# Performance work log

Measured on AMD Instinct MI355X. Metric: run time of the kernel, lower is better.

Reference implementation:

```python
import jax, jax.numpy as jnp
import numpy as np

NUM_TREES = 150
ARITY = 4
DEPTH = 4
NUM_LEVELS = DEPTH + 1  # leaves (level 0) ... root (level DEPTH)
VOCAB = 10000
SUBTOK = 8
EMB_DIM = 256
HID = 256
NUM_CLASSES = 2


def _build_forest():
    # perfect ARITY-ary tree, level-order indexing; edges point child -> parent
    n = (ARITY ** (DEPTH + 1) - 1) // (ARITY - 1)  # 341
    src = np.arange(1, n)
    dst = (src - 1) // ARITY
    depth_of = np.zeros(n, dtype=np.int64)
    for j in range(1, n):
        depth_of[j] = depth_of[(j - 1) // ARITY] + 1
    level_of = DEPTH - depth_of  # leaves = 0, processed first (topo order)
    offs = np.arange(NUM_TREES) * n
    edge_src = (src[None, :] + offs[:, None]).ravel().astype(np.int32)
    edge_dst = (dst[None, :] + offs[:, None]).ravel().astype(np.int32)
    node_level = np.tile(level_of, NUM_TREES).astype(np.int32)
    graph_id = np.repeat(np.arange(NUM_TREES), n).astype(np.int32)
    leaf_mask = (node_level == 0).astype(np.int32)
    return edge_src, edge_dst, node_level, graph_id, leaf_mask, NUM_TREES * n


def setup_inputs() -> dict:
    key = jax.random.key(0)
    ks = jax.random.split(key, 16)
    es, ed, lvl, gid, lm, N = _build_forest()
    s_e = 1.0 / np.sqrt(EMB_DIM)
    s_h = 1.0 / np.sqrt(HID)
    s_f = 1.0 / np.sqrt(2 * HID)
    return {
        "node_feat1": jax.random.randint(ks[0], (N, SUBTOK), 0, VOCAB, dtype=jnp.int32),
        "node_feat2": jax.random.randint(ks[1], (N, SUBTOK), 0, VOCAB, dtype=jnp.int32),
        "emb1": jax.random.normal(ks[2], (VOCAB, EMB_DIM), jnp.float32) * 0.02,
        "emb2": jax.random.normal(ks[3], (VOCAB, EMB_DIM), jnp.float32) * 0.02,
        "W_iou1": jax.random.normal(ks[4], (EMB_DIM, 3 * HID), jnp.float32) * s_e,
        "W_iou2": jax.random.normal(ks[5], (EMB_DIM, 3 * HID), jnp.float32) * s_e,
        "U_iou1": jax.random.normal(ks[6], (HID, 3 * HID), jnp.float32) * s_h,
        "U_iou2": jax.random.normal(ks[7], (HID, 3 * HID), jnp.float32) * s_h,
        "Uf_W1": jax.random.normal(ks[8], (HID, HID), jnp.float32) * s_h,
        "Uf_b1": jnp.zeros((HID,), jnp.float32),
        "Uf_W2": jax.random.normal(ks[9], (HID, HID), jnp.float32) * s_h,
        "Uf_b2": jnp.zeros((HID,), jnp.float32),
        "b_iou1": jnp.zeros((3 * HID,), jnp.float32),
        "b_iou2": jnp.zeros((3 * HID,), jnp.float32),
        "Wf": jax.random.normal(ks[10], (2 * HID, NUM_CLASSES), jnp.float32) * s_f,
        "bf": jnp.zeros((NUM_CLASSES,), jnp.float32),
        "edge_src": jnp.asarray(es),
        "edge_dst": jnp.asarray(ed),
        "node_level": jnp.asarray(lvl),
        "graph_id": jnp.asarray(gid),
        "leaf_mask": jnp.asarray(lm),
    }


def _tree_lstm(iou0, U_iou, Uf_W, Uf_b, b_iou, edge_src, edge_dst, node_level):
    # ChildSum TreeLSTM, propagated level-by-level (leaves -> root)
    N = iou0.shape[0]
    h = jnp.zeros((N, HID), iou0.dtype)
    c = jnp.zeros((N, HID), iou0.dtype)
    for lvl in range(NUM_LEVELS):
        emask = (node_level[edge_dst] == lvl).astype(h.dtype)[:, None]  # [E,1]
        hs = h[edge_src] * emask  # children h (already computed at lower levels)
        f = jax.nn.sigmoid(hs @ Uf_W + Uf_b)  # per-edge forget gate
        h_tild = jax.ops.segment_sum(hs, edge_dst, num_segments=N)
        c_sum = jax.ops.segment_sum(f * c[edge_src] * emask, edge_dst, num_segments=N)
        has_child = jax.ops.segment_sum(emask, edge_dst, num_segments=N) > 0  # [N,1]
        # DGL semantics: reduce overwrites iou for internal nodes; leaves keep W_iou(x)*mask
        iou = jnp.where(has_child, h_tild @ U_iou, iou0) + b_iou
        i, o, u = jnp.split(iou, 3, axis=1)
        c_new = jax.nn.sigmoid(i) * jnp.tanh(u) + c_sum
        h_new = jax.nn.sigmoid(o) * jnp.tanh(c_new)
        at = (node_level == lvl)[:, None]
        h = jnp.where(at, h_new, h)
        c = jnp.where(at, c_new, c)
    return h


def _branch(node_feat, emb, W_iou, U_iou, Uf_W, Uf_b, b_iou,
            leaf_mask, edge_src, edge_dst, node_level, graph_id):
    embeds = emb[node_feat].mean(axis=1)  # subtoken mean pooling -> [N, EMB_DIM]
    iou0 = (embeds @ W_iou) * leaf_mask.astype(embeds.dtype)[:, None]
    h = _tree_lstm(iou0, U_iou, Uf_W, Uf_b, b_iou, edge_src, edge_dst, node_level)
    s = jax.ops.segment_sum(h, graph_id, num_segments=NUM_TREES)
    cnt = jax.ops.segment_sum(jnp.ones((h.shape[0],), h.dtype), graph_id, num_segments=NUM_TREES)
    return jax.nn.relu(s / cnt[:, None])  # mean graph readout + relu


def reference(node_feat1, node_feat2, emb1, emb2, W_iou1, W_iou2, U_iou1, U_iou2,
              Uf_W1, Uf_b1, Uf_W2, Uf_b2, b_iou1, b_iou2, Wf, bf,
              edge_src, edge_dst, node_level, graph_id, leaf_mask):
    m1 = _branch(node_feat1, emb1, W_iou1, U_iou1, Uf_W1, Uf_b1, b_iou1,
                 leaf_mask, edge_src, edge_dst, node_level, graph_id)
    m2 = _branch(node_feat2, emb2, W_iou2, U_iou2, Uf_W2, Uf_b2, b_iou2,
                 leaf_mask, edge_src, edge_dst, node_level, graph_id)
    logits = jax.nn.leaky_relu(jnp.concatenate([m1, m2], axis=1) @ Wf + bf, 0.01)
    return jax.nn.softmax(logits, axis=-1)
```

## Files before the change

kernel.cpp:

```cpp
#include <hip/hip_runtime.h>

#define NT 150
#define NPT 341
#define LEAF0 85
#define NL (NT*256)
#define NN (NT*NPT)
#define VOCAB 10000

typedef __attribute__((ext_vector_type(8))) short short8;
typedef __attribute__((ext_vector_type(4))) float floatx4;

__device__ __forceinline__ float sigf(float x){ return 1.0f/(1.0f+__expf(-x)); }
__device__ __forceinline__ float bf2f(ushort u){ union{unsigned i; float f;} v; v.i = ((unsigned)u)<<16; return v.f; }
__device__ __forceinline__ ushort f2bf(float x){ union{float f; unsigned i;} v; v.f = x; return (ushort)((v.i + 0x7fff + ((v.i>>16)&1))>>16); }

__global__ __launch_bounds__(256) void convW_k(
    const float* __restrict__ W1, const float* __restrict__ U1, const float* __restrict__ F1,
    const float* __restrict__ W2, const float* __restrict__ U2, const float* __restrict__ F2,
    ushort* Wt1, ushort* Ut1, ushort* Ft1, ushort* Wt2, ushort* Ut2, ushort* Ft2){
  __shared__ float T[32][33];
  const float* src; ushort* dst; int N;
  switch (blockIdx.z){
    case 0: src=W1; dst=Wt1; N=768; break;
    case 1: src=U1; dst=Ut1; N=768; break;
    case 2: src=F1; dst=Ft1; N=256; break;
    case 3: src=W2; dst=Wt2; N=768; break;
    case 4: src=U2; dst=Ut2; N=768; break;
    default: src=F2; dst=Ft2; N=256; break;
  }
  int n0 = blockIdx.x*32; if (n0 >= N) return;
  int k0 = blockIdx.y*32;
  int nl = threadIdx.x & 31, kb = threadIdx.x >> 5;
  #pragma unroll
  for (int i=0;i<4;i++){ int kk = kb*4+i; T[kk][nl] = src[(size_t)(k0+kk)*N + n0 + nl]; }
  __syncthreads();
  #pragma unroll
  for (int i=0;i<4;i++){ int nn = kb*4+i; dst[(size_t)(n0+nn)*256 + k0 + nl] = f2bf(T[nl][nn]); }
}

__global__ __launch_bounds__(256) void convE_k(
    const float* __restrict__ e1, const float* __restrict__ e2,
    ushort* __restrict__ E1, ushort* __restrict__ E2){
  const float* s = blockIdx.y ? e2 : e1;
  ushort* d = blockIdx.y ? E2 : E1;
  size_t i = ((size_t)blockIdx.x*256 + threadIdx.x)*4;
  float4 v = *(const float4*)&s[i];
  d[i+0]=f2bf(v.x); d[i+1]=f2bf(v.y); d[i+2]=f2bf(v.z); d[i+3]=f2bf(v.w);
}

__global__ __launch_bounds__(256) void embed_k(
    const int* __restrict__ f1, const int* __restrict__ f2,
    const ushort* __restrict__ E1, const ushort* __restrict__ E2,
    ushort* __restrict__ h1, ushort* __restrict__ h2){
  int br = blockIdx.y;
  const int* feat = br ? f2 : f1;
  const ushort* E = br ? E2 : E1;
  ushort* h = br ? h2 : h1;
  int t = threadIdx.x;
  int leaf = blockIdx.x*16 + (t>>4);
  int seg = t & 15;
  int tree = leaf >> 8;
  size_t node = (size_t)tree*NPT + LEAF0 + (leaf & 255);
  const int* f = feat + node*8;
  float s[16];
  #pragma unroll
  for (int q=0;q<16;q++) s[q]=0.f;
  #pragma unroll
  for (int j=0;j<8;j++){
    const ushort* row = E + (size_t)f[j]*256 + seg*16;
    short8 a = *(const short8*)row;
    short8 b = *(const short8*)(row+8);
    #pragma unroll
    for (int q=0;q<8;q++){ s[q]+=bf2f((ushort)a[q]); s[8+q]+=bf2f((ushort)b[q]); }
  }
  short8 o1, o2;
  #pragma unroll
  for (int q=0;q<8;q++){ o1[q]=(short)f2bf(s[q]*0.125f); o2[q]=(short)f2bf(s[8+q]*0.125f); }
  ushort* dst = h + node*256 + seg*16;
  *(short8*)dst = o1; *(short8*)(dst+8) = o2;
}

__global__ __launch_bounds__(1024) void leaf_gemm(
    const ushort* __restrict__ Wt1, const float* __restrict__ b1,
    const ushort* __restrict__ Wt2, const float* __restrict__ b2,
    ushort* __restrict__ h1, ushort* __restrict__ c1,
    ushort* __restrict__ h2, ushort* __restrict__ c2){
  __shared__ __attribute__((aligned(16))) ushort As[8][64*40];
  int br = blockIdx.y;
  const ushort* Wt = br ? Wt2 : Wt1;
  const float* biou = br ? b2 : b1;
  ushort* h = br ? h2 : h1;
  ushort* c = br ? c2 : c1;
  int tid = threadIdx.x;
  int lane = tid & 63, wav = tid >> 6, quad = lane >> 4, l15 = lane & 15;
  int rowbase = blockIdx.x*64;

  {
    int row = tid >> 4, seg = tid & 15;
    int leaf = rowbase + row;
    int tree = leaf >> 8;
    size_t node = (size_t)tree*NPT + LEAF0 + (leaf & 255);
    const ushort* src = h + node*256 + seg*16;
    short8 a = *(const short8*)src;
    short8 b = *(const short8*)(src+8);
    int cch = seg >> 1, off = (seg & 1)*16;
    *(short8*)&As[cch][row*40 + off]     = a;
    *(short8*)&As[cch][row*40 + off + 8] = b;
  }
  __syncthreads();

  floatx4 acc[3][4];
  #pragma unroll
  for (int g=0;g<3;g++)
    #pragma unroll
    for (int r=0;r<4;r++) acc[g][r] = (floatx4){0.f,0.f,0.f,0.f};

  const ushort* bp0 = Wt + (size_t)(0*256 + wav*16 + l15)*256 + quad*8;
  const ushort* bp1 = Wt + (size_t)(1*256 + wav*16 + l15)*256 + quad*8;
  const ushort* bp2 = Wt + (size_t)(2*256 + wav*16 + l15)*256 + quad*8;

  #pragma unroll
  for (int cch=0; cch<8; cch++){
    short8 b0 = *(const short8*)(bp0 + cch*32);
    short8 b1 = *(const short8*)(bp1 + cch*32);
    short8 b2 = *(const short8*)(bp2 + cch*32);
    #pragma unroll
    for (int r=0;r<4;r++){
      short8 a = *(const short8*)&As[cch][(16*r + l15)*40 + quad*8];
      acc[0][r] = __builtin_amdgcn_mfma_f32_16x16x32_bf16(a, b0, acc[0][r], 0,0,0);
      acc[1][r] = __builtin_amdgcn_mfma_f32_16x16x32_bf16(a, b1, acc[1][r], 0,0,0);
      acc[2][r] = __builtin_amdgcn_mfma_f32_16x16x32_bf16(a, b2, acc[2][r], 0,0,0);
    }
  }
  int hc = wav*16 + l15;
  float bi = biou[hc], bo = biou[256+hc], bu = biou[512+hc];
  #pragma unroll
  for (int r=0;r<4;r++){
    #pragma unroll
    for (int reg=0;reg<4;reg++){
      int leaf = rowbase + 16*r + quad*4 + reg;
      int tree = leaf >> 8;
      size_t node = (size_t)tree*NPT + LEAF0 + (leaf & 255);
      float iv = acc[0][r][reg] + bi;
      float ov = acc[1][r][reg] + bo;
      float uv = acc[2][r][reg] + bu;
      float cc = sigf(iv)*tanhf(uv);
      float hh = sigf(ov)*tanhf(cc);
      h[node*256 + hc] = f2bf(hh);
      c[node*256 + hc] = f2bf(cc);
    }
  }
}

__global__ __launch_bounds__(256) void level_k(
    const ushort* __restrict__ Ut1, const ushort* __restrict__ Ft1,
    const float* __restrict__ Ufb1, const float* __restrict__ bi1,
    const ushort* __restrict__ Ut2, const ushort* __restrict__ Ft2,
    const float* __restrict__ Ufb2, const float* __restrict__ bi2,
    ushort* __restrict__ h1, ushort* __restrict__ c1,
    ushort* __restrict__ h2, ushort* __restrict__ c2,
    int M, int shift, int base){
  __shared__ __attribute__((aligned(16))) ushort Ch[8][64*40];
  __shared__ __attribute__((aligned(16))) ushort Ht[8][16*40];
  __shared__ float Cs[16*68];
  int br = blockIdx.z;
  const ushort* Ut = br ? Ut2 : Ut1;
  const ushort* Ft = br ? Ft2 : Ft1;
  const float* Ufb = br ? Ufb2 : Ufb1;
  const float* biou = br ? bi2 : bi1;
  ushort* h = br ? h2 : h1;
  ushort* c = br ? c2 : c1;
  int tid = threadIdx.x;
  int lane = tid & 63, wav = tid >> 6, quad = lane >> 4, l15 = lane & 15;
  int m0 = blockIdx.x*16, cb = blockIdx.y;
  int mask = (1<<shift)-1;

  {
    int cl = tid >> 2, q4 = tid & 3;
    int sm = m0 + (cl >> 2); if (sm > M-1) sm = M-1;
    int stree = sm >> shift, sloc = base + (sm & mask);
    const ushort* sgp = h + ((size_t)stree*NPT + 4*sloc + 1 + (cl & 3))*256 + q4*8;
    #pragma unroll
    for (int cc=0;cc<8;cc++)
      *(short8*)&Ch[cc][cl*40 + q4*8] = *(const short8*)(sgp + cc*32);
  }
  __syncthreads();
  {
    int n = tid & 15, hcki = tid >> 4;
    int cc = hcki >> 1, off = (hcki & 1)*16;
    float s[16];
    #pragma unroll
    for (int q=0;q<16;q++) s[q]=0.f;
    #pragma unroll
    for (int i=0;i<4;i++){
      short8 a = *(const short8*)&Ch[cc][(4*n+i)*40 + off];
      short8 b = *(const short8*)&Ch[cc][(4*n+i)*40 + off + 8];
      #pragma unroll
      for (int q=0;q<8;q++){ s[q]+=bf2f((ushort)a[q]); s[8+q]+=bf2f((ushort)b[q]); }
    }
    short8 o1,o2;
    #pragma unroll
    for (int q=0;q<8;q++){ o1[q]=(short)f2bf(s[q]); o2[q]=(short)f2bf(s[8+q]); }
    *(short8*)&Ht[cc][n*40 + off]     = o1;
    *(short8*)&Ht[cc][n*40 + off + 8] = o2;
  }
  __syncthreads();

  const ushort* bfp = Ft + (size_t)(cb*64 + wav*16 + l15)*256 + quad*8;
  const ushort* bp0 = Ut + (size_t)(0*256 + cb*64 + wav*16 + l15)*256 + quad*8;
  const ushort* bp1 = Ut + (size_t)(1*256 + cb*64 + wav*16 + l15)*256 + quad*8;
  const ushort* bp2 = Ut + (size_t)(2*256 + cb*64 + wav*16 + l15)*256 + quad*8;

  floatx4 accf[4], acci[3];
  #pragma unroll
  for (int r=0;r<4;r++) accf[r] = (floatx4){0.f,0.f,0.f,0.f};
  #pragma unroll
  for (int g=0;g<3;g++) acci[g] = (floatx4){0.f,0.f,0.f,0.f};

  #pragma unroll
  for (int cc=0; cc<8; cc++){
    short8 bfw = *(const short8*)(bfp + cc*32);
    short8 b0 = *(const short8*)(bp0 + cc*32);
    short8 b1 = *(const short8*)(bp1 + cc*32);
    short8 b2 = *(const short8*)(bp2 + cc*32);
    short8 ah = *(const short8*)&Ht[cc][l15*40 + quad*8];
    #pragma unroll
    for (int r=0;r<4;r++){
      short8 a = *(const short8*)&Ch[cc][(16*r + l15)*40 + quad*8];
      accf[r] = __builtin_amdgcn_mfma_f32_16x16x32_bf16(a, bfw, accf[r], 0,0,0);
    }
    acci[0] = __builtin_amdgcn_mfma_f32_16x16x32_bf16(ah, b0, acci[0], 0,0,0);
    acci[1] = __builtin_amdgcn_mfma_f32_16x16x32_bf16(ah, b1, acci[1], 0,0,0);
    acci[2] = __builtin_amdgcn_mfma_f32_16x16x32_bf16(ah, b2, acci[2], 0,0,0);
  }

  int hc = cb*64 + wav*16 + l15;
  float ufb = Ufb[hc];
  #pragma unroll
  for (int r=0;r<4;r++){
    int ni = 4*r + quad;
    int m = m0 + ni; if (m > M-1) m = M-1;
    int tree = m >> shift, loc = base + (m & mask);
    size_t chbase = ((size_t)tree*NPT + 4*loc + 1)*256 + hc;
    float cs = 0.f;
    #pragma unroll
    for (int reg=0;reg<4;reg++)
      cs += sigf(accf[r][reg] + ufb) * bf2f(c[chbase + (size_t)reg*256]);
    Cs[ni*68 + wav*16 + l15] = cs;
  }
  __syncthreads();
  float bi = biou[hc], bo = biou[256+hc], bu = biou[512+hc];
  #pragma unroll
  for (int reg=0;reg<4;reg++){
    int ni = quad*4 + reg;
    int m = m0 + ni;
    if (m < M){
      int tree = m >> shift, loc = base + (m & mask);
      size_t off = ((size_t)tree*NPT + loc)*256 + hc;
      float cs = Cs[ni*68 + wav*16 + l15];
      float iv = acci[0][reg] + bi;
      float ov = acci[1][reg] + bo;
      float uv = acci[2][reg] + bu;
      float cn = sigf(iv)*tanhf(uv) + cs;
      float hn = sigf(ov)*tanhf(cn);
      h[off] = f2bf(hn);
      c[off] = f2bf(cn);
    }
  }
}

__global__ __launch_bounds__(256) void readout_k(
    const ushort* __restrict__ h1, const ushort* __restrict__ h2,
    float* __restrict__ m1, float* __restrict__ m2){
  int br = blockIdx.y;
  const ushort* h = br ? h2 : h1;
  float* mo = br ? m2 : m1;
  int tree = blockIdx.x; int t = threadIdx.x;
  const ushort* hp = h + (size_t)tree*NPT*256 + t;
  float s0=0.f,s1=0.f,s2=0.f,s3=0.f;
  for (int i=0; i<340; i+=4){
    s0 += bf2f(hp[(size_t)(i+0)*256]); s1 += bf2f(hp[(size_t)(i+1)*256]);
    s2 += bf2f(hp[(size_t)(i+2)*256]); s3 += bf2f(hp[(size_t)(i+3)*256]);
  }
  float s = s0+s1+s2+s3 + bf2f(hp[(size_t)340*256]);
  mo[tree*256+t] = fmaxf(s*(1.0f/341.0f), 0.f);
}

__global__ __launch_bounds__(64) void final_k(const float* __restrict__ m1,
    const float* __restrict__ m2, const float* __restrict__ Wf,
    const float* __restrict__ bf, float* __restrict__ out){
  int tree = blockIdx.x; int t = threadIdx.x;
  float p0=0.f, p1=0.f;
  for (int k=t;k<512;k+=64){
    float x = (k<256) ? m1[tree*256+k] : m2[tree*256+(k-256)];
    p0 += x*Wf[k*2+0]; p1 += x*Wf[k*2+1];
  }
  #pragma unroll
  for (int off=32; off>0; off>>=1){
    p0 += __shfl_down(p0, off);
    p1 += __shfl_down(p1, off);
  }
  if (t==0){
    float l0 = p0+bf[0], l1 = p1+bf[1];
    l0 = (l0>0.f)?l0:0.01f*l0;
    l1 = (l1>0.f)?l1:0.01f*l1;
    float mx = fmaxf(l0,l1);
    float e0 = __expf(l0-mx), e1 = __expf(l1-mx);
    float inv = 1.0f/(e0+e1);
    out[tree*2+0] = e0*inv; out[tree*2+1] = e1*inv;
  }
}

extern "C" void kernel_launch(void* const* d_in, const int* in_sizes, int n_in,
                              void* d_out, int out_size, void* d_ws, size_t ws_size,
                              hipStream_t stream) {
  const int*   feat1 = (const int*)  d_in[0];
  const int*   feat2 = (const int*)  d_in[1];
  const float* emb1  = (const float*)d_in[2];
  const float* emb2  = (const float*)d_in[3];
  const float* Wiou1 = (const float*)d_in[4];
  const float* Wiou2 = (const float*)d_in[5];
  const float* Uiou1 = (const float*)d_in[6];
  const float* Uiou2 = (const float*)d_in[7];
  const float* UfW1  = (const float*)d_in[8];
  const float* Ufb1  = (const float*)d_in[9];
  const float* UfW2  = (const float*)d_in[10];
  const float* Ufb2  = (const float*)d_in[11];
  const float* biou1 = (const float*)d_in[12];
  const float* biou2 = (const float*)d_in[13];
  const float* Wf    = (const float*)d_in[14];
  const float* bfv   = (const float*)d_in[15];
  float* out = (float*)d_out;

  char* ws = (char*)d_ws;
  ushort* h1  = (ushort*)ws;  ws += (size_t)NN*256*2;
  ushort* h2  = (ushort*)ws;  ws += (size_t)NN*256*2;
  ushort* c1  = (ushort*)ws;  ws += (size_t)NN*256*2;
  ushort* c2  = (ushort*)ws;  ws += (size_t)NN*256*2;
  ushort* E1  = (ushort*)ws;  ws += (size_t)VOCAB*256*2;
  ushort* E2  = (ushort*)ws;  ws += (size_t)VOCAB*256*2;
  ushort* Wt1 = (ushort*)ws;  ws += 768*256*2;
  ushort* Ut1 = (ushort*)ws;  ws += 768*256*2;
  ushort* Ft1 = (ushort*)ws;  ws += 256*256*2;
  ushort* Wt2 = (ushort*)ws;  ws += 768*256*2;
  ushort* Ut2 = (ushort*)ws;  ws += 768*256*2;
  ushort* Ft2 = (ushort*)ws;  ws += 256*256*2;
  float*  m1  = (float*)ws;   ws += NT*256*4;
  float*  m2  = (float*)ws;   ws += NT*256*4;

  convW_k<<<dim3(24, 8, 6), 256, 0, stream>>>(Wiou1, Uiou1, UfW1, Wiou2, Uiou2, UfW2,
                                              Wt1, Ut1, Ft1, Wt2, Ut2, Ft2);
  convE_k<<<dim3(2500, 2), 256, 0, stream>>>(emb1, emb2, E1, E2);
  embed_k<<<dim3(NL/16, 2), 256, 0, stream>>>(feat1, feat2, E1, E2, h1, h2);
  leaf_gemm<<<dim3(NL/64, 2), 1024, 0, stream>>>(Wt1, biou1, Wt2, biou2, h1, c1, h2, c2);

  const int lvlM[4]     = {9600, 2400, 600, 150};
  const int lvlShift[4] = {6, 4, 2, 0};
  const int lvlBase[4]  = {21, 5, 1, 0};
  for (int l=0;l<4;l++){
    int gx = (lvlM[l] + 15)/16;
    level_k<<<dim3(gx, 4, 2), 256, 0, stream>>>(Ut1, Ft1, Ufb1, biou1,
                                                Ut2, Ft2, Ufb2, biou2,
                                                h1, c1, h2, c2,
                                                lvlM[l], lvlShift[l], lvlBase[l]);
  }
  readout_k<<<dim3(NT, 2), 256, 0, stream>>>(h1, h2, m1, m2);
  final_k<<<NT, 64, 0, stream>>>(m1, m2, Wf, bfv, out);
}
```

Baseline: 406.3 us.

## Fold child-sum into MFMA accumulators and split readout into partial sums

The level kernel no longer sums child hidden states into a shared bf16 buffer. It multiplies each child's h directly by the i/o/u weights and adds the four per-child results from the accumulator lanes. This removes a shared-memory pass and two barriers at the cost of four times the MFMA work for the iou gates. The readout is split into four partial chunks per tree for more blocks, and the final kernel sums the partials before the mean and relu.

```diff
diff --git a/kernel.cpp b/kernel.cpp
--- a/kernel.cpp
+++ b/kernel.cpp
@@ -161,8 +161,6 @@
     ushort* __restrict__ h2, ushort* __restrict__ c2,
     int M, int shift, int base){
   __shared__ __attribute__((aligned(16))) ushort Ch[8][64*40];
-  __shared__ __attribute__((aligned(16))) ushort Ht[8][16*40];
-  __shared__ float Cs[16*68];
   int br = blockIdx.z;
   const ushort* Ut = br ? Ut2 : Ut1;
   const ushort* Ft = br ? Ft2 : Ft1;
@@ -185,84 +183,55 @@
       *(short8*)&Ch[cc][cl*40 + q4*8] = *(const short8*)(sgp + cc*32);
   }
   __syncthreads();
-  {
-    int n = tid & 15, hcki = tid >> 4;
-    int cc = hcki >> 1, off = (hcki & 1)*16;
-    float s[16];
-    #pragma unroll
-    for (int q=0;q<16;q++) s[q]=0.f;
-    #pragma unroll
-    for (int i=0;i<4;i++){
-      short8 a = *(const short8*)&Ch[cc][(4*n+i)*40 + off];
-      short8 b = *(const short8*)&Ch[cc][(4*n+i)*40 + off + 8];
-      #pragma unroll
-      for (int q=0;q<8;q++){ s[q]+=bf2f((ushort)a[q]); s[8+q]+=bf2f((ushort)b[q]); }
-    }
-    short8 o1,o2;
-    #pragma unroll
-    for (int q=0;q<8;q++){ o1[q]=(short)f2bf(s[q]); o2[q]=(short)f2bf(s[8+q]); }
-    *(short8*)&Ht[cc][n*40 + off]     = o1;
-    *(short8*)&Ht[cc][n*40 + off + 8] = o2;
-  }
-  __syncthreads();
-
-  const ushort* bfp = Ft + (size_t)(cb*64 + wav*16 + l15)*256 + quad*8;
-  const ushort* bp0 = Ut + (size_t)(0*256 + cb*64 + wav*16 + l15)*256 + quad*8;
-  const ushort* bp1 = Ut + (size_t)(1*256 + cb*64 + wav*16 + l15)*256 + quad*8;
-  const ushort* bp2 = Ut + (size_t)(2*256 + cb*64 + wav*16 + l15)*256 + quad*8;
-
-  floatx4 accf[4], acci[3];
-  #pragma unroll
-  for (int r=0;r<4;r++) accf[r] = (floatx4){0.f,0.f,0.f,0.f};
-  #pragma unroll
-  for (int g=0;g<3;g++) acci[g] = (floatx4){0.f,0.f,0.f,0.f};
+
+  int col = cb*64 + wav*16 + l15;
+  const ushort* bfp = Ft + (size_t)col*256 + quad*8;
+  const ushort* bp0 = Ut + (size_t)(0*256 + col)*256 + quad*8;
+  const ushort* bp1 = Ut + (size_t)(256 + col)*256 + quad*8;
+  const ushort* bp2 = Ut + (size_t)(512 + col)*256 + quad*8;
+
+  floatx4 af[4], ai[4], ao[4], au[4];
+  #pragma unroll
+  for (int r=0;r<4;r++){
+    af[r] = (floatx4){0.f,0.f,0.f,0.f}; ai[r] = (floatx4){0.f,0.f,0.f,0.f};
+    ao[r] = (floatx4){0.f,0.f,0.f,0.f}; au[r] = (floatx4){0.f,0.f,0.f,0.f};
+  }
 
   #pragma unroll
   for (int cc=0; cc<8; cc++){
-    short8 bfw = *(const short8*)(bfp + cc*32);
-    short8 b0 = *(const short8*)(bp0 + cc*32);
-    short8 b1 = *(const short8*)(bp1 + cc*32);
-    short8 b2 = *(const short8*)(bp2 + cc*32);
-    short8 ah = *(const short8*)&Ht[cc][l15*40 + quad*8];
+    short8 Bf = *(const short8*)(bfp + cc*32);
+    short8 Bi = *(const short8*)(bp0 + cc*32);
+    short8 Bo = *(const short8*)(bp1 + cc*32);
+    short8 Bu = *(const short8*)(bp2 + cc*32);
     #pragma unroll
     for (int r=0;r<4;r++){
       short8 a = *(const short8*)&Ch[cc][(16*r + l15)*40 + quad*8];
-      accf[r] = __builtin_amdgcn_mfma_f32_16x16x32_bf16(a, bfw, accf[r], 0,0,0);
+      af[r] = __builtin_amdgcn_mfma_f32_16x16x32_bf16(a, Bf, af[r], 0,0,0);
+      ai[r] = __builtin_amdgcn_mfma_f32_16x16x32_bf16(a, Bi, ai[r], 0,0,0);
+      ao[r] = __builtin_amdgcn_mfma_f32_16x16x32_bf16(a, Bo, ao[r], 0,0,0);
+      au[r] = __builtin_amdgcn_mfma_f32_16x16x32_bf16(a, Bu, au[r], 0,0,0);
     }
-    acci[0] = __builtin_amdgcn_mfma_f32_16x16x32_bf16(ah, b0, acci[0], 0,0,0);
-    acci[1] = __builtin_amdgcn_mfma_f32_16x16x32_bf16(ah, b1, acci[1], 0,0,0);
-    acci[2] = __builtin_amdgcn_mfma_f32_16x16x32_bf16(ah, b2, acci[2], 0,0,0);
-  }
-
-  int hc = cb*64 + wav*16 + l15;
-  float ufb = Ufb[hc];
+  }
+
+  float ufb = Ufb[col];
+  float bI = biou[col], bO = biou[256+col], bU = biou[512+col];
   #pragma unroll
   for (int r=0;r<4;r++){
-    int ni = 4*r + quad;
-    int m = m0 + ni; if (m > M-1) m = M-1;
-    int tree = m >> shift, loc = base + (m & mask);
-    size_t chbase = ((size_t)tree*NPT + 4*loc + 1)*256 + hc;
+    int m = m0 + 4*r + quad;
+    int mm = m < M ? m : M-1;
+    int tree = mm >> shift, loc = base + (mm & mask);
+    size_t ch0 = ((size_t)tree*NPT + 4*loc + 1)*256 + col;
     float cs = 0.f;
     #pragma unroll
     for (int reg=0;reg<4;reg++)
-      cs += sigf(accf[r][reg] + ufb) * bf2f(c[chbase + (size_t)reg*256]);
-    Cs[ni*68 + wav*16 + l15] = cs;
-  }
-  __syncthreads();
-  float bi = biou[hc], bo = biou[256+hc], bu = biou[512+hc];
-  #pragma unroll
-  for (int reg=0;reg<4;reg++){
-    int ni = quad*4 + reg;
-    int m = m0 + ni;
+      cs += sigf(af[r][reg] + ufb) * bf2f(c[ch0 + (size_t)reg*256]);
+    float iv = ai[r][0]+ai[r][1]+ai[r][2]+ai[r][3] + bI;
+    float ov = ao[r][0]+ao[r][1]+ao[r][2]+ao[r][3] + bO;
+    float uv = au[r][0]+au[r][1]+au[r][2]+au[r][3] + bU;
+    float cn = sigf(iv)*tanhf(uv) + cs;
+    float hn = sigf(ov)*tanhf(cn);
     if (m < M){
-      int tree = m >> shift, loc = base + (m & mask);
-      size_t off = ((size_t)tree*NPT + loc)*256 + hc;
-      float cs = Cs[ni*68 + wav*16 + l15];
-      float iv = acci[0][reg] + bi;
-      float ov = acci[1][reg] + bo;
-      float uv = acci[2][reg] + bu;
-      float cn = sigf(iv)*tanhf(uv) + cs;
-      float hn = sigf(ov)*tanhf(cn);
+      size_t off = ((size_t)tree*NPT + loc)*256 + col;
       h[off] = f2bf(hn);
       c[off] = f2bf(cn);
     }
@@ -271,28 +240,35 @@
 
 __global__ __launch_bounds__(256) void readout_k(
     const ushort* __restrict__ h1, const ushort* __restrict__ h2,
-    float* __restrict__ m1, float* __restrict__ m2){
-  int br = blockIdx.y;
+    float* __restrict__ mp1, float* __restrict__ mp2){
+  int br = blockIdx.z, part = blockIdx.y, tree = blockIdx.x;
   const ushort* h = br ? h2 : h1;
-  float* mo = br ? m2 : m1;
-  int tree = blockIdx.x; int t = threadIdx.x;
-  const ushort* hp = h + (size_t)tree*NPT*256 + t;
+  float* mp = br ? mp2 : mp1;
+  int t = threadIdx.x;
+  int start = part*85;
+  int cnt = (part==3) ? 86 : 85;
+  const ushort* hp = h + ((size_t)tree*NPT + start)*256 + t;
   float s0=0.f,s1=0.f,s2=0.f,s3=0.f;
-  for (int i=0; i<340; i+=4){
+  int i = 0;
+  for (; i+4<=cnt; i+=4){
     s0 += bf2f(hp[(size_t)(i+0)*256]); s1 += bf2f(hp[(size_t)(i+1)*256]);
     s2 += bf2f(hp[(size_t)(i+2)*256]); s3 += bf2f(hp[(size_t)(i+3)*256]);
   }
-  float s = s0+s1+s2+s3 + bf2f(hp[(size_t)340*256]);
-  mo[tree*256+t] = fmaxf(s*(1.0f/341.0f), 0.f);
-}
-
-__global__ __launch_bounds__(64) void final_k(const float* __restrict__ m1,
-    const float* __restrict__ m2, const float* __restrict__ Wf,
+  for (; i<cnt; i++) s0 += bf2f(hp[(size_t)i*256]);
+  mp[((size_t)tree*4 + part)*256 + t] = s0+s1+s2+s3;
+}
+
+__global__ __launch_bounds__(64) void final_k(const float* __restrict__ mp1,
+    const float* __restrict__ mp2, const float* __restrict__ Wf,
     const float* __restrict__ bf, float* __restrict__ out){
   int tree = blockIdx.x; int t = threadIdx.x;
   float p0=0.f, p1=0.f;
   for (int k=t;k<512;k+=64){
-    float x = (k<256) ? m1[tree*256+k] : m2[tree*256+(k-256)];
+    const float* mp = (k<256) ? mp1 : mp2;
+    int kk = k & 255;
+    size_t b0 = ((size_t)tree*4)*256 + kk;
+    float s = mp[b0] + mp[b0+256] + mp[b0+512] + mp[b0+768];
+    float x = fmaxf(s*(1.0f/341.0f), 0.f);
     p0 += x*Wf[k*2+0]; p1 += x*Wf[k*2+1];
   }
   #pragma unroll
@@ -345,8 +321,8 @@
   ushort* Wt2 = (ushort*)ws;  ws += 768*256*2;
   ushort* Ut2 = (ushort*)ws;  ws += 768*256*2;
   ushort* Ft2 = (ushort*)ws;  ws += 256*256*2;
-  float*  m1  = (float*)ws;   ws += NT*256*4;
-  float*  m2  = (float*)ws;   ws += NT*256*4;
+  float*  mp1 = (float*)ws;   ws += (size_t)NT*4*256*4;
+  float*  mp2 = (float*)ws;   ws += (size_t)NT*4*256*4;
 
   convW_k<<<dim3(24, 8, 6), 256, 0, stream>>>(Wiou1, Uiou1, UfW1, Wiou2, Uiou2, UfW2,
                                               Wt1, Ut1, Ft1, Wt2, Ut2, Ft2);
@@ -364,6 +340,6 @@
                                                 h1, c1, h2, c2,
                                                 lvlM[l], lvlShift[l], lvlBase[l]);
   }
-  readout_k<<<dim3(NT, 2), 256, 0, stream>>>(h1, h2, m1, m2);
-  final_k<<<NT, 64, 0, stream>>>(m1, m2, Wf, bfv, out);
-}
+  readout_k<<<dim3(NT, 4, 2), 256, 0, stream>>>(h1, h2, mp1, mp2);
+  final_k<<<NT, 64, 0, stream>>>(mp1, mp2, Wf, bfv, out);
+}
```

Result: faster. 380.8 us (-6.3%).
